# Optimization experiments

Measured on AMD Instinct MI355X. Metric: run time of the kernel, lower is better.

Reference implementation:

```python
import jax, jax.numpy as jnp
import numpy as np

PC_RANGE = (-54.0, -54.0, -5.0, 54.0, 54.0, 3.0)
VOXEL = (0.075, 0.075, 0.2)
STRIDE = 8
FW = 180  # feature map size along x
FH = 180  # feature map size along y
NUM_CLASS = 2
M = 500   # num_max_objs
MIN_RADIUS = 2
OVERLAP = 0.1
C_IN = 128
HM_C = 2
REG_C = 9
B = 4


def conv2d(x, w, b=None):
    y = jax.lax.conv_general_dilated(x, w, (1, 1), 'SAME',
                                     dimension_numbers=('NCHW', 'OIHW', 'NCHW'))
    return y if b is None else y + b[None, :, None, None]


def bn(x, g, b, m, v, eps=1e-5):
    inv = g / jnp.sqrt(v + eps)
    return x * inv[None, :, None, None] + (b - m * inv)[None, :, None, None]


def gaussian_radius(height, width, min_overlap):
    # centernet_utils.gaussian_radius
    b1 = height + width
    c1 = width * height * (1.0 - min_overlap) / (1.0 + min_overlap)
    r1 = (b1 + jnp.sqrt(jnp.maximum(b1 * b1 - 4.0 * c1, 0.0))) / 2.0
    b2 = 2.0 * (height + width)
    c2 = (1.0 - min_overlap) * width * height
    r2 = (b2 + jnp.sqrt(jnp.maximum(b2 * b2 - 16.0 * c2, 0.0))) / 2.0
    a3 = 4.0 * min_overlap
    b3 = -2.0 * min_overlap * (height + width)
    c3 = (min_overlap - 1.0) * width * height
    r3 = (b3 + jnp.sqrt(jnp.maximum(b3 * b3 - 4.0 * a3 * c3, 0.0))) / (2.0 * a3)
    return jnp.minimum(jnp.minimum(r1, r2), r3)


def assign_targets(gt):
    # gt: (B, M, 8) = [x, y, z, dx, dy, dz, ry, cls]; cls==0 / zero box = padding
    x, y, z = gt[..., 0], gt[..., 1], gt[..., 2]
    dx, dy, dz, ry = gt[..., 3], gt[..., 4], gt[..., 5], gt[..., 6]
    cls = gt[..., 7].astype(jnp.int32)
    coord_x = jnp.clip((x - PC_RANGE[0]) / VOXEL[0] / STRIDE, 0.0, FW - 0.5)
    coord_y = jnp.clip((y - PC_RANGE[1]) / VOXEL[1] / STRIDE, 0.0, FH - 0.5)
    cxi = coord_x.astype(jnp.int32)
    cyi = coord_y.astype(jnp.int32)
    dxp = dx / VOXEL[0] / STRIDE
    dyp = dy / VOXEL[1] / STRIDE
    radius = jnp.maximum(gaussian_radius(dxp, dyp, OVERLAP).astype(jnp.int32), MIN_RADIUS)
    valid = (dxp > 0) & (dyp > 0)
    pos = valid & (cls >= 1)

    # --- dense gaussian splat, max-reduced per class (= draw_gaussian_to_heatmap) ---
    ddx = jnp.arange(FW)[None, None, :] - cxi[..., None]   # (B,M,FW)
    ddy = jnp.arange(FH)[None, None, :] - cyi[..., None]   # (B,M,FH)
    sigma = (2.0 * radius.astype(jnp.float32) + 1.0) / 6.0
    d2 = (ddy[..., :, None] ** 2 + ddx[..., None, :] ** 2).astype(jnp.float32)  # (B,M,FH,FW)
    g = jnp.exp(-d2 / (2.0 * sigma[..., None, None] ** 2))
    win = (jnp.abs(ddy) <= radius[..., None])[..., :, None] & \
          (jnp.abs(ddx) <= radius[..., None])[..., None, :]
    g = jnp.where(win & pos[..., None, None], g, 0.0)
    seg = jnp.where(pos, cls - 1, NUM_CLASS)
    hmv = jax.vmap(lambda gv, sv: jax.ops.segment_max(gv, sv, num_segments=NUM_CLASS + 1))(
        g.reshape(B, M, FH * FW), seg)
    heatmap = jnp.maximum(hmv[:, :NUM_CLASS].reshape(B, NUM_CLASS, FH, FW), 0.0)
    heatmap_mask = (heatmap > 0).astype(gt.dtype)

    # --- inds / mask / ret_boxes (5 slots per object: center + 4 neighbors) ---
    base_ind = cyi * FW + cxi
    w_cond = VOXEL[0] * STRIDE > dy / 4.0   # faithful: uses temp_w = gt[:,4]
    l_cond = VOXEL[1] * STRIDE > dx / 4.0   # faithful: uses temp_l = gt[:,3]
    left = cxi - 1 >= 0
    right = cxi + 1 < FW
    up = cyi - 1 >= 0
    down = cyi + 1 < FH
    m0 = jnp.where(valid, jnp.where(cls >= 1, 1, -1), 0)
    s1 = valid & ~w_cond & left
    s2 = valid & ~w_cond & right
    s3 = valid & ~l_cond & up
    s4 = valid & ~l_cond & down
    mask = jnp.stack([m0,
                      jnp.where(s1, m0, 0), jnp.where(s2, m0, 0),
                      jnp.where(s3, m0, 0), jnp.where(s4, m0, 0)], -1).reshape(B, 5 * M)
    inds = jnp.stack([jnp.where(valid, base_ind, 0),
                      jnp.where(s1, base_ind - 1, 0), jnp.where(s2, base_ind + 1, 0),
                      jnp.where(s3, base_ind - FW, 0), jnp.where(s4, base_ind + FW, 0)],
                     -1).reshape(B, 5 * M).astype(jnp.int32)
    offx = coord_x - cxi.astype(gt.dtype)
    offy = coord_y - cyi.astype(gt.dtype)
    base = jnp.stack([offx, offy, z,
                      jnp.log(jnp.maximum(dx, 1e-8)),
                      jnp.log(jnp.maximum(dy, 1e-8)),
                      jnp.log(jnp.maximum(dz, 1e-8)),
                      jnp.cos(ry), jnp.sin(ry)], -1)          # (B,M,8)
    z5 = jnp.zeros((B, M), gt.dtype)
    dx_adj = jnp.stack([z5, s1.astype(gt.dtype), -s2.astype(gt.dtype), z5, z5], -1)  # (B,M,5)
    dy_adj = jnp.stack([z5, z5, z5, s3.astype(gt.dtype), -s4.astype(gt.dtype)], -1)
    zero5 = jnp.zeros_like(dx_adj)
    delta = jnp.stack([dx_adj, dy_adj, zero5, zero5, zero5, zero5, zero5, zero5], -1)  # (B,M,5,8)
    rb = (base[:, :, None, :] + delta) * valid[:, :, None, None].astype(gt.dtype)
    ret_boxes = rb.reshape(B, 5 * M, 8)
    return heatmap, ret_boxes, inds, mask, heatmap_mask


def setup_inputs():
    key = jax.random.key(0)
    ks = jax.random.split(key, 12)
    x = jax.random.normal(ks[0], (B, C_IN, FH, FW), jnp.float32)
    # realistic gt boxes; last 150 per scene are zero padding
    cxy = jax.random.uniform(ks[1], (B, M, 2), minval=-50.0, maxval=50.0)
    zc = jax.random.uniform(ks[2], (B, M, 1), minval=-2.0, maxval=1.0)
    dims = jax.random.uniform(ks[3], (B, M, 3), minval=0.5, maxval=6.0)
    ry = jax.random.uniform(ks[4], (B, M, 1), minval=-3.14, maxval=3.14)
    cls = jax.random.randint(ks[5], (B, M, 1), 1, NUM_CLASS + 1).astype(jnp.float32)
    vm = (jnp.arange(M) < 350)[None, :, None].astype(jnp.float32)
    gt_boxes = jnp.concatenate([cxy, zc, dims, ry, cls], -1) * vm
    p = lambda k, s, sc: jax.random.normal(k, s, jnp.float32) * sc
    return {
        'x': x, 'gt_boxes': gt_boxes,
        'conv1_w': p(ks[6], (C_IN, C_IN, 3, 3), 0.02),
        'bn1_g': jnp.ones((C_IN,)), 'bn1_b': jnp.zeros((C_IN,)),
        'bn1_m': jnp.zeros((C_IN,)), 'bn1_v': jnp.ones((C_IN,)),
        'conv2_w': p(ks[7], (C_IN, C_IN, 3, 3), 0.02),
        'bn2_g': jnp.ones((C_IN,)), 'bn2_b': jnp.zeros((C_IN,)),
        'bn2_m': jnp.zeros((C_IN,)), 'bn2_v': jnp.ones((C_IN,)),
        'hm_w': p(ks[8], (HM_C, C_IN, 3, 3), 0.02),
        'hm_b': jnp.full((HM_C,), -2.19, jnp.float32),
        'reg_w': p(ks[9], (REG_C, C_IN, 3, 3), 0.001),
        'reg_b': jnp.zeros((REG_C,), jnp.float32),
    }


def reference(x, gt_boxes, conv1_w, bn1_g, bn1_b, bn1_m, bn1_v,
              conv2_w, bn2_g, bn2_b, bn2_m, bn2_v, hm_w, hm_b, reg_w, reg_b):
    f = jax.nn.relu(bn(conv2d(x, conv1_w), bn1_g, bn1_b, bn1_m, bn1_v))
    f = jax.nn.relu(bn(conv2d(f, conv2_w), bn2_g, bn2_b, bn2_m, bn2_v))
    hm = conv2d(f, hm_w, hm_b)      # (B, 2, H, W)
    reg = conv2d(f, reg_w, reg_b)   # (B, 9, H, W)
    heatmap, ret_boxes, inds, mask, heatmap_mask = assign_targets(gt_boxes)
    return hm, reg, heatmap, ret_boxes, inds, mask, heatmap_mask
```

## Files before the change

kernel.cpp:

```cpp
#include <hip/hip_runtime.h>
#include <math.h>

typedef unsigned short u16;
typedef short bf16x8 __attribute__((ext_vector_type(8)));
typedef float f32x4 __attribute__((ext_vector_type(4)));

#define FW_ 180
#define FH_ 180
#define HW_ (FW_*FH_)
#define CIN_ 128
#define BB_ 4
#define MM_ 500
#define PW_ 182
#define PADE ((size_t)BB_*PW_*PW_*CIN_)

#define HM_OFF   0
#define REG_OFF  (BB_*2*HW_)
#define HEAT_OFF (REG_OFF + BB_*9*HW_)
#define RB_OFF   (HEAT_OFF + BB_*2*HW_)
#define IND_OFF  (RB_OFF + BB_*MM_*5*8)
#define MSK_OFF  (IND_OFF + BB_*MM_*5)
#define HMM_OFF  (MSK_OFF + BB_*MM_*5)

__device__ inline u16 f2bf(float f) {
    unsigned u = __float_as_uint(f);
    u += 0x7FFFu + ((u >> 16) & 1u);
    return (u16)(u >> 16);
}

#define GLOAD_LDS16(gsrc, ldst) \
    __builtin_amdgcn_global_load_lds( \
        (const __attribute__((address_space(1))) unsigned*)(gsrc), \
        (__attribute__((address_space(3))) unsigned*)(ldst), 16, 0, 0)

__global__ void k_init_w(u16* __restrict__ ws, float* __restrict__ out,
                         const float* __restrict__ w1, const float* __restrict__ w2,
                         const float* __restrict__ hw, const float* __restrict__ rw,
                         u16* __restrict__ wT1, u16* __restrict__ wT2,
                         u16* __restrict__ wTh)
{
    int idx = blockIdx.x * 256 + threadIdx.x;
    const int n1 = 3 * BB_ * PW_ * PW_;
    const int n2 = n1 + BB_ * 2 * HW_;
    const int NW = 9 * CIN_ * CIN_;
    const int n3 = n2 + NW;
    const int n4 = n3 + NW;
    const int n5 = n4 + 9 * 16 * CIN_;
    if (idx < n1) {
        int buf = idx / (BB_ * PW_ * PW_);
        int rem = idx % (BB_ * PW_ * PW_);
        int p = rem % (PW_ * PW_);
        int r = p / PW_, c = p % PW_;
        if (r > 0 && r < PW_ - 1 && c > 0 && c < PW_ - 1) return;
        u16* base = ws + (size_t)buf * PADE + (size_t)rem * CIN_;
#pragma unroll
        for (int i = 0; i < 16; ++i) ((uint4*)base)[i] = make_uint4(0, 0, 0, 0);
    } else if (idx < n2) {
        out[HEAT_OFF + (idx - n1)] = 0.f;
    } else if (idx < n3) {
        int j = idx - n2;
        int tap = j / (CIN_ * CIN_);
        int r = j % (CIN_ * CIN_);
        int co = r >> 7, ci = r & 127;
        wT1[j] = f2bf(w1[((size_t)co * CIN_ + ci) * 9 + tap]);
    } else if (idx < n4) {
        int j = idx - n3;
        int tap = j / (CIN_ * CIN_);
        int r = j % (CIN_ * CIN_);
        int co = r >> 7, ci = r & 127;
        wT2[j] = f2bf(w2[((size_t)co * CIN_ + ci) * 9 + tap]);
    } else if (idx < n5) {
        int j = idx - n4;
        int tap = j / (16 * CIN_);
        int r = j % (16 * CIN_);
        int co = r >> 7, ci = r & 127;
        float v = 0.f;
        if (co < 2)       v = hw[((size_t)co * CIN_ + ci) * 9 + tap];
        else if (co < 11) v = rw[((size_t)(co - 2) * CIN_ + ci) * 9 + tap];
        wTh[j] = f2bf(v);
    }
}

__global__ __launch_bounds__(256) void k_prep_xT(const float* __restrict__ in,
                                                 u16* __restrict__ xT)
{
    __shared__ unsigned lt32[180 * 65];
    int tid = threadIdx.x;
    int row = blockIdx.x, b = blockIdx.y;
    const float* inr = in + ((size_t)b * CIN_ * FH_ + row) * FW_;
    for (int i = tid; i < 64 * 45; i += 256) {
        int ci2 = i / 45, c4 = i - 45 * ci2;
        const float* p0 = inr + (size_t)(2 * ci2) * HW_ + c4 * 4;
        float4 a = *(const float4*)p0;
        float4 bq = *(const float4*)(p0 + HW_);
        lt32[(c4 * 4 + 0) * 65 + ci2] = (unsigned)f2bf(a.x) | ((unsigned)f2bf(bq.x) << 16);
        lt32[(c4 * 4 + 1) * 65 + ci2] = (unsigned)f2bf(a.y) | ((unsigned)f2bf(bq.y) << 16);
        lt32[(c4 * 4 + 2) * 65 + ci2] = (unsigned)f2bf(a.z) | ((unsigned)f2bf(bq.z) << 16);
        lt32[(c4 * 4 + 3) * 65 + ci2] = (unsigned)f2bf(a.w) | ((unsigned)f2bf(bq.w) << 16);
    }
    __syncthreads();
    unsigned* dst = (unsigned*)(xT + ((size_t)b * PW_ * PW_ + (size_t)(row + 1) * PW_ + 1) * CIN_);
    for (int idx = tid; idx < 180 * 16; idx += 256) {
        int col = idx >> 4, q = idx & 15;
        uint4 v;
        v.x = lt32[col * 65 + q * 4 + 0];
        v.y = lt32[col * 65 + q * 4 + 1];
        v.z = lt32[col * 65 + q * 4 + 2];
        v.w = lt32[col * 65 + q * 4 + 3];
        *(uint4*)&dst[col * 64 + q * 4] = v;
    }
}

__global__ __launch_bounds__(256, 4) void k_conv_v10(
    const u16* __restrict__ xT, const u16* __restrict__ wT,
    const float* __restrict__ gg, const float* __restrict__ bbn,
    const float* __restrict__ mmn, const float* __restrict__ vvn,
    u16* __restrict__ yT)
{
    __shared__ u16 lin[1600 * 8];
    __shared__ u16 lwt[768 * 8];

    int tid  = threadIdx.x;
    int wv   = tid >> 6, lane = tid & 63;
    int lm   = lane & 15, hi = lane >> 4;
    int csp  = blockIdx.x % 3, cog = blockIdx.x / 3;
    int C0   = (csp == 2) ? 116 : csp * 64;
    int cob  = cog * 64;
    int R0   = blockIdx.y * 4;
    int b    = blockIdx.z;
    const u16* xb = xT + (size_t)b * PW_ * PW_ * CIN_;

    f32x4 acc[4][4];
#pragma unroll
    for (int i = 0; i < 4; ++i)
#pragma unroll
        for (int j = 0; j < 4; ++j) acc[i][j] = (f32x4){0.f, 0.f, 0.f, 0.f};

    unsigned soffI[6];
#pragma unroll
    for (int rd = 0; rd < 6; ++rd) {
        int o = rd * 256 + tid;
        int rc = o >> 2;
        int r = rc / 66, c = rc - 66 * r;
        int q = (o & 3) ^ ((c >> 1) & 3);
        soffI[rd] = (unsigned)(((R0 + r) * PW_ + (C0 + c)) * CIN_ + q * 8);
    }
    unsigned soffX = 0;
    if (tid < 64) {
        int o = 1536 + tid;
        int rc = o >> 2;
        int r = rc / 66, c = rc - 66 * r;
        if (o >= 1584) { r = 5; c = 65; }
        int q = (o & 3) ^ ((c >> 1) & 3);
        soffX = (unsigned)(((R0 + r) * PW_ + (C0 + c)) * CIN_ + q * 8);
    }
    const int wco = tid >> 2;
    const int wq  = (tid & 3) ^ ((wco >> 1) & 3);
    const unsigned soffW = (unsigned)((cob + wco) * CIN_ + wq * 8);

#pragma unroll 1
    for (int ch = 0; ch < 4; ++ch) {
        const int ci0 = ch * 32;
#pragma unroll
        for (int tg = 0; tg < 3; ++tg) {
            __syncthreads();
            if (tg == 0) {
#pragma unroll
                for (int rd = 0; rd < 6; ++rd)
                    GLOAD_LDS16(xb + soffI[rd] + ci0, &lin[(size_t)(rd * 256 + wv * 64) * 8]);
                if (tid < 64)
                    GLOAD_LDS16(xb + soffX + ci0, &lin[(size_t)1536 * 8]);
            }
#pragma unroll
            for (int rd = 0; rd < 3; ++rd)
                GLOAD_LDS16(wT + (size_t)(tg * 3 + rd) * CIN_ * CIN_ + soffW + ci0,
                            &lwt[(size_t)(rd * 256 + wv * 64) * 8]);
            __syncthreads();

#pragma unroll
            for (int t = 0; t < 3; ++t) {
                bf16x8 av[4];
#pragma unroll
                for (int mf = 0; mf < 4; ++mf) {
                    int col = mf * 16 + lm;
                    int unit = t * 256 + col * 4 + (hi ^ ((col >> 1) & 3));
                    av[mf] = *(const bf16x8*)&lwt[(size_t)unit * 8];
                }
#pragma unroll
                for (int nf = 0; nf < 4; ++nf) {
                    int c = wv * 16 + lm + t;
                    int rc = (nf + tg) * 66 + c;
                    int unit = rc * 4 + (hi ^ ((c >> 1) & 3));
                    bf16x8 bv = *(const bf16x8*)&lin[(size_t)unit * 8];
#pragma unroll
                    for (int mf = 0; mf < 4; ++mf)
                        acc[mf][nf] = __builtin_amdgcn_mfma_f32_16x16x32_bf16(
                            av[mf], bv, acc[mf][nf], 0, 0, 0);
                }
            }
        }
    }

#pragma unroll
    for (int mf = 0; mf < 4; ++mf) {
        int co0 = cob + mf * 16 + hi * 4;
        float4 g4 = *(const float4*)(gg + co0);
        float4 b4 = *(const float4*)(bbn + co0);
        float4 m4 = *(const float4*)(mmn + co0);
        float4 v4 = *(const float4*)(vvn + co0);
        float sc0 = g4.x / sqrtf(v4.x + 1e-5f), sh0 = b4.x - m4.x * sc0;
        float sc1 = g4.y / sqrtf(v4.y + 1e-5f), sh1 = b4.y - m4.y * sc1;
        float sc2 = g4.z / sqrtf(v4.z + 1e-5f), sh2 = b4.z - m4.z * sc2;
        float sc3 = g4.w / sqrtf(v4.w + 1e-5f), sh3 = b4.w - m4.w * sc3;
#pragma unroll
        for (int nf = 0; nf < 4; ++nf) {
            f32x4 A = acc[mf][nf];
            float y0 = fmaxf(fmaf(A[0], sc0, sh0), 0.f);
            float y1 = fmaxf(fmaf(A[1], sc1, sh1), 0.f);
            float y2 = fmaxf(fmaf(A[2], sc2, sh2), 0.f);
            float y3 = fmaxf(fmaf(A[3], sc3, sh3), 0.f);
            unsigned p0 = (unsigned)f2bf(y0) | ((unsigned)f2bf(y1) << 16);
            unsigned p1 = (unsigned)f2bf(y2) | ((unsigned)f2bf(y3) << 16);
            u16* op = yT + (size_t)b * PW_ * PW_ * CIN_ +
                      ((size_t)(R0 + nf + 1) * PW_ + (C0 + wv * 16 + lm + 1)) * CIN_ + co0;
            *(uint2*)op = make_uint2(p0, p1);
        }
    }
}

__global__ __launch_bounds__(256) void k_head_v9(
    const u16* __restrict__ f2T, const u16* __restrict__ wTh,
    const float* __restrict__ hb, const float* __restrict__ rb,
    float* __restrict__ out)
{
    __shared__ u16 lin[1600 * 8];
    __shared__ u16 lwt[2304 * 8];

    int tid  = threadIdx.x;
    int wv   = tid >> 6, lane = tid & 63;
    int lm   = lane & 15, hi = lane >> 4;
    int csp  = blockIdx.x;
    int C0   = (csp == 2) ? 116 : csp * 64;
    int R0   = blockIdx.y * 4;
    int b    = blockIdx.z;
    const u16* xb = f2T + (size_t)b * PW_ * PW_ * CIN_;

    f32x4 acc[4];
#pragma unroll
    for (int i = 0; i < 4; ++i) acc[i] = (f32x4){0.f, 0.f, 0.f, 0.f};

#pragma unroll
    for (int rd = 0; rd < 9; ++rd) {
        int o = rd * 256 + tid;
        int tap = o >> 8, rest = o & 255;
        int co = rest >> 4, u8s = rest & 15;
        const u16* src = wTh + (size_t)tap * 16 * CIN_ + co * CIN_ + ((u8s ^ (co & 7)) * 8);
        GLOAD_LDS16(src, &lwt[(size_t)(rd * 256 + wv * 64) * 8]);
    }

#pragma unroll 1
    for (int ch = 0; ch < 4; ++ch) {
        int ci0 = ch * 32;
        __syncthreads();
#pragma unroll
        for (int rd = 0; rd < 6; ++rd) {
            int o = rd * 256 + tid;
            int rc = o >> 2;
            int r = rc / 66, c = rc - 66 * r;
            int q = (o & 3) ^ ((c >> 1) & 3);
            const u16* src = xb + ((size_t)(R0 + r) * PW_ + (C0 + c)) * CIN_ + ci0 + q * 8;
            GLOAD_LDS16(src, &lin[(size_t)(rd * 256 + wv * 64) * 8]);
        }
        if (tid < 64) {
            int o = 1536 + tid;
            int rc = o >> 2;
            int r = rc / 66, c = rc - 66 * r;
            if (o >= 1584) { r = 5; c = 65; }
            int q = (o & 3) ^ ((c >> 1) & 3);
            const u16* src = xb + ((size_t)(R0 + r) * PW_ + (C0 + c)) * CIN_ + ci0 + q * 8;
            GLOAD_LDS16(src, &lin[(size_t)1536 * 8]);
        }
        __syncthreads();

#pragma unroll
        for (int tap = 0; tap < 9; ++tap) {
            const int kr = tap / 3, kc = tap - 3 * (tap / 3);
            int u8 = (ch * 4 + hi) ^ (lm & 7);
            bf16x8 av = *(const bf16x8*)&lwt[(size_t)(tap * 256 + lm * 16 + u8) * 8];
#pragma unroll
            for (int nf = 0; nf < 4; ++nf) {
                int c = wv * 16 + lm + kc;
                int rc = (nf + kr) * 66 + c;
                int unit = rc * 4 + (hi ^ ((c >> 1) & 3));
                bf16x8 bv = *(const bf16x8*)&lin[(size_t)unit * 8];
                acc[nf] = __builtin_amdgcn_mfma_f32_16x16x32_bf16(av, bv, acc[nf], 0, 0, 0);
            }
        }
    }

#pragma unroll
    for (int nf = 0; nf < 4; ++nf) {
        int row = R0 + nf, col = C0 + wv * 16 + lm;
        f32x4 A = acc[nf];
#pragma unroll
        for (int r = 0; r < 4; ++r) {
            int co = hi * 4 + r;
            float v = A[r];
            if (co < 2)
                out[HM_OFF + ((size_t)(b * 2 + co)) * HW_ + (size_t)row * FW_ + col] = v + hb[co];
            else if (co < 11)
                out[REG_OFF + ((size_t)(b * 9 + co - 2)) * HW_ + (size_t)row * FW_ + col] = v + rb[co - 2];
        }
    }

    int blk = (b * 45 + (int)blockIdx.y) * 3 + csp;
    int base = blk * 480;
    for (int i = base + tid; i < base + 480; i += 256) {
        float v = out[HEAT_OFF + i];
        out[HMM_OFF + i] = v > 0.f ? 1.f : 0.f;
    }
}

__global__ void k_objects(const float* __restrict__ gt, float* __restrict__ out)
{
    int ob = blockIdx.x;
    int b = ob / MM_, m = ob % MM_;
    const float* gp = gt + (size_t)ob * 8;
    float x = gp[0], y = gp[1], z = gp[2];
    float dx = gp[3], dy = gp[4], dz = gp[5], ry = gp[6];
    int cls = (int)gp[7];

    float coord_x = fminf(fmaxf((x + 54.f) / 0.075f / 8.f, 0.f), 179.5f);
    float coord_y = fminf(fmaxf((y + 54.f) / 0.075f / 8.f, 0.f), 179.5f);
    int cxi = (int)coord_x, cyi = (int)coord_y;
    float dxp = dx / 0.075f / 8.f;
    float dyp = dy / 0.075f / 8.f;

    float hgt = dxp, wid = dyp, mo = 0.1f;
    float b1 = hgt + wid, c1 = wid * hgt * (1.f - mo) / (1.f + mo);
    float r1 = (b1 + sqrtf(fmaxf(b1 * b1 - 4.f * c1, 0.f))) * 0.5f;
    float b2 = 2.f * (hgt + wid), c2 = (1.f - mo) * wid * hgt;
    float r2 = (b2 + sqrtf(fmaxf(b2 * b2 - 16.f * c2, 0.f))) * 0.5f;
    float a3 = 4.f * mo, b3 = -2.f * mo * (hgt + wid), c3 = (mo - 1.f) * wid * hgt;
    float r3 = (b3 + sqrtf(fmaxf(b3 * b3 - 4.f * a3 * c3, 0.f))) / (2.f * a3);
    int radius = max((int)fminf(fminf(r1, r2), r3), 2);

    bool valid = (dxp > 0.f) && (dyp > 0.f);
    bool pos = valid && (cls >= 1);

    if (threadIdx.x == 0) {
        float m0 = valid ? (cls >= 1 ? 1.f : -1.f) : 0.f;
        bool w_cond = (0.075f * 8.f) > dy / 4.f;
        bool l_cond = (0.075f * 8.f) > dx / 4.f;
        bool s1 = valid && !w_cond && (cxi - 1 >= 0);
        bool s2 = valid && !w_cond && (cxi + 1 < FW_);
        bool s3 = valid && !l_cond && (cyi - 1 >= 0);
        bool s4 = valid && !l_cond && (cyi + 1 < FH_);
        int base_ind = cyi * FW_ + cxi;

        float* indp = out + IND_OFF + (size_t)b * MM_ * 5 + m * 5;
        float* mskp = out + MSK_OFF + (size_t)b * MM_ * 5 + m * 5;
        indp[0] = valid ? (float)base_ind : 0.f;
        indp[1] = s1 ? (float)(base_ind - 1) : 0.f;
        indp[2] = s2 ? (float)(base_ind + 1) : 0.f;
        indp[3] = s3 ? (float)(base_ind - FW_) : 0.f;
        indp[4] = s4 ? (float)(base_ind + FW_) : 0.f;
        mskp[0] = m0;
        mskp[1] = s1 ? m0 : 0.f;
        mskp[2] = s2 ? m0 : 0.f;
        mskp[3] = s3 ? m0 : 0.f;
        mskp[4] = s4 ? m0 : 0.f;

        float offx = coord_x - (float)cxi;
        float offy = coord_y - (float)cyi;
        float bse[8] = { offx, offy, z,
                         logf(fmaxf(dx, 1e-8f)), logf(fmaxf(dy, 1e-8f)),
                         logf(fmaxf(dz, 1e-8f)), cosf(ry), sinf(ry) };
        float vm = valid ? 1.f : 0.f;
        float* rbp = out + RB_OFF + ((size_t)b * MM_ + m) * 5 * 8;
#pragma unroll
        for (int s = 0; s < 5; ++s) {
            float t0 = bse[0], t1 = bse[1];
            if (s == 1) t0 += s1 ? 1.f : 0.f;
            if (s == 2) t0 -= s2 ? 1.f : 0.f;
            if (s == 3) t1 += s3 ? 1.f : 0.f;
            if (s == 4) t1 -= s4 ? 1.f : 0.f;
            rbp[s * 8 + 0] = t0 * vm;
            rbp[s * 8 + 1] = t1 * vm;
#pragma unroll
            for (int k = 2; k < 8; ++k) rbp[s * 8 + k] = bse[k] * vm;
        }
    }

    if (pos) {
        float sigma = (2.f * (float)radius + 1.f) / 6.f;
        float inv2s2 = 1.f / (2.f * sigma * sigma);
        int x0 = max(cxi - radius, 0), x1 = min(cxi + radius, FW_ - 1);
        int y0 = max(cyi - radius, 0), y1 = min(cyi + radius, FH_ - 1);
        int wdt = x1 - x0 + 1, tot = wdt * (y1 - y0 + 1);
        float* hp = out + HEAT_OFF + (size_t)(b * 2 + (cls - 1)) * HW_;
        for (int i = threadIdx.x; i < tot; i += blockDim.x) {
            int yy = y0 + i / wdt, xx = x0 + i % wdt;
            float ddy = (float)(yy - cyi), ddx = (float)(xx - cxi);
            float gvl = expf(-(ddy * ddy + ddx * ddx) * inv2s2);
            atomicMax((int*)(hp + yy * FW_ + xx), __float_as_int(gvl));
        }
    }
}

extern "C" void kernel_launch(void* const* d_in, const int* in_sizes, int n_in,
                              void* d_out, int out_size, void* d_ws, size_t ws_size,
                              hipStream_t stream)
{
    const float* x  = (const float*)d_in[0];
    const float* gt = (const float*)d_in[1];
    const float* w1 = (const float*)d_in[2];
    const float* g1 = (const float*)d_in[3];
    const float* b1 = (const float*)d_in[4];
    const float* m1 = (const float*)d_in[5];
    const float* v1 = (const float*)d_in[6];
    const float* w2 = (const float*)d_in[7];
    const float* g2 = (const float*)d_in[8];
    const float* b2 = (const float*)d_in[9];
    const float* m2 = (const float*)d_in[10];
    const float* v2 = (const float*)d_in[11];
    const float* hw = (const float*)d_in[12];
    const float* hb = (const float*)d_in[13];
    const float* rw = (const float*)d_in[14];
    const float* rb = (const float*)d_in[15];
    float* out = (float*)d_out;

    u16* ws  = (u16*)d_ws;
    u16* xT  = ws;
    u16* f1T = ws + PADE;
    u16* f2T = ws + 2 * PADE;
    u16* wT1 = ws + 3 * PADE;
    u16* wT2 = wT1 + 9 * CIN_ * CIN_;
    u16* wTh = wT2 + 9 * CIN_ * CIN_;

    const int NTOT = 3 * BB_ * PW_ * PW_ + BB_ * 2 * HW_
                   + 2 * 9 * CIN_ * CIN_ + 9 * 16 * CIN_;
    k_init_w<<<(NTOT + 255) / 256, 256, 0, stream>>>(ws, out, w1, w2, hw, rw,
                                                     wT1, wT2, wTh);
    k_prep_xT<<<dim3(180, BB_), 256, 0, stream>>>(x, xT);
    k_objects<<<BB_ * MM_, 64, 0, stream>>>(gt, out);

    dim3 cg(6, 45, BB_);
    k_conv_v10<<<cg, 256, 0, stream>>>(xT,  wT1, g1, b1, m1, v1, f1T);
    k_conv_v10<<<cg, 256, 0, stream>>>(f1T, wT2, g2, b2, m2, v2, f2T);

    dim3 hg(3, 45, BB_);
    k_head_v9<<<hg, 256, 0, stream>>>(f2T, wTh, hb, rb, out);
}
```

Baseline: 156.6 us.

## Double-buffer conv LDS tiles with prefetch and remap workgroups across XCDs

The 3x3 conv kernel now keeps two LDS buffers for both the input tile and the weight tile. It issues the global-to-LDS loads for the next tap-group or channel chunk before computing on the current buffer, so only one barrier is needed per step instead of two. The 3D grid becomes a flat grid of 1080 blocks, with the block index swizzled so that neighbouring tiles land on the same XCD for better L2 reuse. The cost is double the LDS use, with launch bounds lowered from 4 to 2 blocks per CU, which reduces occupancy. Correctness also depends on the async LDS loads being complete at the barrier.

New measurement: 152.5 us. -2.6%, faster.

```diff
diff --git a/kernel.cpp b/kernel.cpp
--- a/kernel.cpp
+++ b/kernel.cpp
@@ -111,23 +111,29 @@
     }
 }
 
-__global__ __launch_bounds__(256, 4) void k_conv_v10(
+__global__ __launch_bounds__(256, 2) void k_conv_v11(
     const u16* __restrict__ xT, const u16* __restrict__ wT,
     const float* __restrict__ gg, const float* __restrict__ bbn,
     const float* __restrict__ mmn, const float* __restrict__ vvn,
     u16* __restrict__ yT)
 {
-    __shared__ u16 lin[1600 * 8];
-    __shared__ u16 lwt[768 * 8];
+    __shared__ u16 lin[2][1600 * 8];
+    __shared__ u16 lwt[2][768 * 8];
 
     int tid  = threadIdx.x;
     int wv   = tid >> 6, lane = tid & 63;
     int lm   = lane & 15, hi = lane >> 4;
-    int csp  = blockIdx.x % 3, cog = blockIdx.x / 3;
+
+    int wg   = blockIdx.x;
+    int wgid = (wg & 7) * 135 + (wg >> 3);
+    int b    = wgid / 270;
+    int rem  = wgid % 270;
+    int row  = rem / 6;
+    int t6   = rem % 6;
+    int csp  = t6 % 3, cog = t6 / 3;
     int C0   = (csp == 2) ? 116 : csp * 64;
     int cob  = cog * 64;
-    int R0   = blockIdx.y * 4;
-    int b    = blockIdx.z;
+    int R0   = row * 4;
     const u16* xb = xT + (size_t)b * PW_ * PW_ * CIN_;
 
     f32x4 acc[4][4];
@@ -158,25 +164,42 @@
     const int wq  = (tid & 3) ^ ((wco >> 1) & 3);
     const unsigned soffW = (unsigned)((cob + wco) * CIN_ + wq * 8);
 
+#pragma unroll
+    for (int rd = 0; rd < 6; ++rd)
+        GLOAD_LDS16(xb + soffI[rd], &lin[0][(size_t)(rd * 256 + wv * 64) * 8]);
+    if (tid < 64) GLOAD_LDS16(xb + soffX, &lin[0][(size_t)1536 * 8]);
+#pragma unroll
+    for (int rd = 0; rd < 3; ++rd)
+        GLOAD_LDS16(wT + (size_t)rd * CIN_ * CIN_ + soffW,
+                    &lwt[0][(size_t)(rd * 256 + wv * 64) * 8]);
+
 #pragma unroll 1
     for (int ch = 0; ch < 4; ++ch) {
-        const int ci0 = ch * 32;
 #pragma unroll
         for (int tg = 0; tg < 3; ++tg) {
             __syncthreads();
-            if (tg == 0) {
-#pragma unroll
-                for (int rd = 0; rd < 6; ++rd)
-                    GLOAD_LDS16(xb + soffI[rd] + ci0, &lin[(size_t)(rd * 256 + wv * 64) * 8]);
-                if (tid < 64)
-                    GLOAD_LDS16(xb + soffX + ci0, &lin[(size_t)1536 * 8]);
+            if (!(ch == 3 && tg == 2)) {
+                const int nch = (tg == 2) ? ch + 1 : ch;
+                const int ntg = (tg == 2) ? 0 : tg + 1;
+                const int nbufW = (nch + ntg) & 1;
+                if (ntg == 0) {
+                    const int nci = nch * 32;
+                    const int nbI = nch & 1;
+#pragma unroll
+                    for (int rd = 0; rd < 6; ++rd)
+                        GLOAD_LDS16(xb + soffI[rd] + nci,
+                                    &lin[nbI][(size_t)(rd * 256 + wv * 64) * 8]);
+                    if (tid < 64)
+                        GLOAD_LDS16(xb + soffX + nci, &lin[nbI][(size_t)1536 * 8]);
+                }
+#pragma unroll
+                for (int rd = 0; rd < 3; ++rd)
+                    GLOAD_LDS16(wT + (size_t)(ntg * 3 + rd) * CIN_ * CIN_ + soffW + nch * 32,
+                                &lwt[nbufW][(size_t)(rd * 256 + wv * 64) * 8]);
             }
-#pragma unroll
-            for (int rd = 0; rd < 3; ++rd)
-                GLOAD_LDS16(wT + (size_t)(tg * 3 + rd) * CIN_ * CIN_ + soffW + ci0,
-                            &lwt[(size_t)(rd * 256 + wv * 64) * 8]);
-            __syncthreads();
-
+
+            const u16* lwtb = lwt[(ch + tg) & 1];
+            const u16* linb = lin[ch & 1];
 #pragma unroll
             for (int t = 0; t < 3; ++t) {
                 bf16x8 av[4];
@@ -184,14 +207,14 @@
                 for (int mf = 0; mf < 4; ++mf) {
                     int col = mf * 16 + lm;
                     int unit = t * 256 + col * 4 + (hi ^ ((col >> 1) & 3));
-                    av[mf] = *(const bf16x8*)&lwt[(size_t)unit * 8];
+                    av[mf] = *(const bf16x8*)&lwtb[(size_t)unit * 8];
                 }
 #pragma unroll
                 for (int nf = 0; nf < 4; ++nf) {
                     int c = wv * 16 + lm + t;
                     int rc = (nf + tg) * 66 + c;
                     int unit = rc * 4 + (hi ^ ((c >> 1) & 3));
-                    bf16x8 bv = *(const bf16x8*)&lin[(size_t)unit * 8];
+                    bf16x8 bv = *(const bf16x8*)&linb[(size_t)unit * 8];
 #pragma unroll
                     for (int mf = 0; mf < 4; ++mf)
                         acc[mf][nf] = __builtin_amdgcn_mfma_f32_16x16x32_bf16(
@@ -445,9 +468,8 @@
     k_prep_xT<<<dim3(180, BB_), 256, 0, stream>>>(x, xT);
     k_objects<<<BB_ * MM_, 64, 0, stream>>>(gt, out);
 
-    dim3 cg(6, 45, BB_);
-    k_conv_v10<<<cg, 256, 0, stream>>>(xT,  wT1, g1, b1, m1, v1, f1T);
-    k_conv_v10<<<cg, 256, 0, stream>>>(f1T, wT2, g2, b2, m2, v2, f2T);
+    k_conv_v11<<<1080, 256, 0, stream>>>(xT,  wT1, g1, b1, m1, v1, f1T);
+    k_conv_v11<<<1080, 256, 0, stream>>>(f1T, wT2, g2, b2, m2, v2, f2T);
 
     dim3 hg(3, 45, BB_);
     k_head_v9<<<hg, 256, 0, stream>>>(f2T, wTh, hb, rb, out);
```

## Pipeline conv weight loads with triple-buffered LDS and XCD-aware block remap

Applied to the files above, without the earlier changes.

The conv kernel now triple-buffers the weight tiles in LDS. It prefetches the next tap-group's weights while the current one computes, and uses explicit vmcnt waits with raw s_barrier instead of two __syncthreads per step. The 3D grid is flattened to 1080 blocks, and block IDs are remapped so that consecutive tiles land on the same XCD, which is meant to improve L2 reuse. The larger LDS footprint, with launch bounds lowered to 2, cuts the number of resident blocks per CU, trading latency hiding through occupancy for software pipelining.

Result: faster. 147.2 us (-6.0%).

```diff
diff --git a/kernel.cpp b/kernel.cpp
--- a/kernel.cpp
+++ b/kernel.cpp
@@ -111,23 +111,29 @@
     }
 }
 
-__global__ __launch_bounds__(256, 4) void k_conv_v10(
+__global__ __launch_bounds__(256, 2) void k_conv_v13(
     const u16* __restrict__ xT, const u16* __restrict__ wT,
     const float* __restrict__ gg, const float* __restrict__ bbn,
     const float* __restrict__ mmn, const float* __restrict__ vvn,
     u16* __restrict__ yT)
 {
     __shared__ u16 lin[1600 * 8];
-    __shared__ u16 lwt[768 * 8];
+    __shared__ u16 lwt[3][768 * 8];
 
     int tid  = threadIdx.x;
     int wv   = tid >> 6, lane = tid & 63;
     int lm   = lane & 15, hi = lane >> 4;
-    int csp  = blockIdx.x % 3, cog = blockIdx.x / 3;
+
+    int wg   = blockIdx.x;
+    int wgid = (wg & 7) * 135 + (wg >> 3);
+    int b    = wgid / 270;
+    int rem  = wgid % 270;
+    int row  = rem / 6;
+    int t6   = rem % 6;
+    int csp  = t6 % 3, cog = t6 / 3;
     int C0   = (csp == 2) ? 116 : csp * 64;
     int cob  = cog * 64;
-    int R0   = blockIdx.y * 4;
-    int b    = blockIdx.z;
+    int R0   = row * 4;
     const u16* xb = xT + (size_t)b * PW_ * PW_ * CIN_;
 
     f32x4 acc[4][4];
@@ -158,48 +164,76 @@
     const int wq  = (tid & 3) ^ ((wco >> 1) & 3);
     const unsigned soffW = (unsigned)((cob + wco) * CIN_ + wq * 8);
 
-#pragma unroll 1
+    #define STAGE_IN(CH)                                                        \
+    {                                                                           \
+        _Pragma("unroll")                                                       \
+        for (int rd = 0; rd < 6; ++rd)                                          \
+            GLOAD_LDS16(xb + soffI[rd] + (CH) * 32,                             \
+                        &lin[(size_t)(rd * 256 + wv * 64) * 8]);                \
+        if (tid < 64)                                                           \
+            GLOAD_LDS16(xb + soffX + (CH) * 32, &lin[(size_t)1536 * 8]);        \
+    }
+    #define STAGE_W(NCH, NTG)                                                   \
+    {                                                                           \
+        _Pragma("unroll")                                                       \
+        for (int rd = 0; rd < 3; ++rd)                                          \
+            GLOAD_LDS16(wT + (size_t)((NTG) * 3 + rd) * CIN_ * CIN_ + soffW + (NCH) * 32, \
+                        &lwt[NTG][(size_t)(rd * 256 + wv * 64) * 8]);           \
+    }
+    #define COMPUTE_TG(TG)                                                      \
+    {                                                                           \
+        _Pragma("unroll")                                                       \
+        for (int t = 0; t < 3; ++t) {                                           \
+            bf16x8 av[4];                                                       \
+            _Pragma("unroll")                                                   \
+            for (int mf = 0; mf < 4; ++mf) {                                    \
+                int col = mf * 16 + lm;                                         \
+                int unit = t * 256 + col * 4 + (hi ^ ((col >> 1) & 3));         \
+                av[mf] = *(const bf16x8*)&lwt[TG][(size_t)unit * 8];            \
+            }                                                                   \
+            _Pragma("unroll")                                                   \
+            for (int nf = 0; nf < 4; ++nf) {                                    \
+                int c = wv * 16 + lm + t;                                       \
+                int rc = (nf + (TG)) * 66 + c;                                  \
+                int unit = rc * 4 + (hi ^ ((c >> 1) & 3));                      \
+                bf16x8 bv = *(const bf16x8*)&lin[(size_t)unit * 8];             \
+                _Pragma("unroll")                                               \
+                for (int mf = 0; mf < 4; ++mf)                                  \
+                    acc[mf][nf] = __builtin_amdgcn_mfma_f32_16x16x32_bf16(      \
+                        av[mf], bv, acc[mf][nf], 0, 0, 0);                      \
+            }                                                                   \
+        }                                                                       \
+    }
+
+    STAGE_IN(0);
+    STAGE_W(0, 0);
+
+#pragma unroll
     for (int ch = 0; ch < 4; ++ch) {
-        const int ci0 = ch * 32;
 #pragma unroll
         for (int tg = 0; tg < 3; ++tg) {
-            __syncthreads();
-            if (tg == 0) {
-#pragma unroll
-                for (int rd = 0; rd < 6; ++rd)
-                    GLOAD_LDS16(xb + soffI[rd] + ci0, &lin[(size_t)(rd * 256 + wv * 64) * 8]);
-                if (tid < 64)
-                    GLOAD_LDS16(xb + soffX + ci0, &lin[(size_t)1536 * 8]);
+            if (tg == 0 && ch > 0) {
+                __builtin_amdgcn_s_barrier();
+                __builtin_amdgcn_sched_barrier(0);
+                STAGE_IN(ch);
             }
-#pragma unroll
-            for (int rd = 0; rd < 3; ++rd)
-                GLOAD_LDS16(wT + (size_t)(tg * 3 + rd) * CIN_ * CIN_ + soffW + ci0,
-                            &lwt[(size_t)(rd * 256 + wv * 64) * 8]);
-            __syncthreads();
-
-#pragma unroll
-            for (int t = 0; t < 3; ++t) {
-                bf16x8 av[4];
-#pragma unroll
-                for (int mf = 0; mf < 4; ++mf) {
-                    int col = mf * 16 + lm;
-                    int unit = t * 256 + col * 4 + (hi ^ ((col >> 1) & 3));
-                    av[mf] = *(const bf16x8*)&lwt[(size_t)unit * 8];
-                }
-#pragma unroll
-                for (int nf = 0; nf < 4; ++nf) {
-                    int c = wv * 16 + lm + t;
-                    int rc = (nf + tg) * 66 + c;
-                    int unit = rc * 4 + (hi ^ ((c >> 1) & 3));
-                    bf16x8 bv = *(const bf16x8*)&lin[(size_t)unit * 8];
-#pragma unroll
-                    for (int mf = 0; mf < 4; ++mf)
-                        acc[mf][nf] = __builtin_amdgcn_mfma_f32_16x16x32_bf16(
-                            av[mf], bv, acc[mf][nf], 0, 0, 0);
-                }
+            const bool last = (ch == 3 && tg == 2);
+            if (!last) {
+                const int nch = (tg == 2) ? ch + 1 : ch;
+                const int ntg = (tg + 1) % 3;
+                STAGE_W(nch, ntg);
+                asm volatile("s_waitcnt vmcnt(3)" ::: "memory");
+            } else {
+                asm volatile("s_waitcnt vmcnt(0)" ::: "memory");
             }
-        }
-    }
+            __builtin_amdgcn_s_barrier();
+            __builtin_amdgcn_sched_barrier(0);
+            COMPUTE_TG(tg);
+        }
+    }
+    #undef STAGE_IN
+    #undef STAGE_W
+    #undef COMPUTE_TG
 
 #pragma unroll
     for (int mf = 0; mf < 4; ++mf) {
@@ -445,9 +479,8 @@
     k_prep_xT<<<dim3(180, BB_), 256, 0, stream>>>(x, xT);
     k_objects<<<BB_ * MM_, 64, 0, stream>>>(gt, out);
 
-    dim3 cg(6, 45, BB_);
-    k_conv_v10<<<cg, 256, 0, stream>>>(xT,  wT1, g1, b1, m1, v1, f1T);
-    k_conv_v10<<<cg, 256, 0, stream>>>(f1T, wT2, g2, b2, m2, v2, f2T);
+    k_conv_v13<<<1080, 256, 0, stream>>>(xT,  wT1, g1, b1, m1, v1, f1T);
+    k_conv_v13<<<1080, 256, 0, stream>>>(f1T, wT2, g2, b2, m2, v2, f2T);
 
     dim3 hg(3, 45, BB_);
     k_head_v9<<<hg, 256, 0, stream>>>(f2T, wTh, hb, rb, out);
```
